# Performance work log

Measured on AMD Instinct MI355X. Metric: run time of the kernel, lower is better.

Reference implementation:

```python
import jax, jax.numpy as jnp
import numpy as np
from jax import lax

N, C, H, W, Q, HD = 2, 64, 96, 96, 147456, 128

def make_coord(h, w):
    # pixel-center coords in [-1,1]; channel 0 -> H dim, channel 1 -> W dim
    y = -1.0 + (2.0 * jnp.arange(h) + 1.0) / h
    x = -1.0 + (2.0 * jnp.arange(w) + 1.0) / w
    yy, xx = jnp.meshgrid(y, x, indexing='ij')
    return jnp.stack([yy, xx], 0)[None]  # [1,2,h,w]

def _pix(c, n):
    # align_corners=False unnormalization
    return ((c + 1.0) * n - 1.0) / 2.0

def gather_nearest(img, cy, cx):
    # img [n,c,h,w]; cy,cx [n,q] in [-1,1] -> [n,q,c]
    n, c, h, w = img.shape
    iy = jnp.clip(jnp.round(_pix(cy, h)).astype(jnp.int32), 0, h - 1)
    ix = jnp.clip(jnp.round(_pix(cx, w)).astype(jnp.int32), 0, w - 1)
    flat = img.reshape(n, c, h * w)
    out = jnp.take_along_axis(flat, (iy * w + ix)[:, None, :], axis=2)
    return out.transpose(0, 2, 1)

def sample_bilinear_border(img, cy, cx):
    # grid_sample bilinear, padding_mode='border', align_corners=False
    n, c, h, w = img.shape
    fy = jnp.clip(_pix(cy, h), 0.0, h - 1.0)
    fx = jnp.clip(_pix(cx, w), 0.0, w - 1.0)
    y0 = jnp.floor(fy); x0 = jnp.floor(fx)
    wy = fy - y0; wx = fx - x0
    y0i = jnp.clip(y0.astype(jnp.int32), 0, h - 1); y1i = jnp.clip(y0i + 1, 0, h - 1)
    x0i = jnp.clip(x0.astype(jnp.int32), 0, w - 1); x1i = jnp.clip(x0i + 1, 0, w - 1)
    flat = img.reshape(n, c, h * w)
    def g(iy, ix):
        return jnp.take_along_axis(flat, (iy * w + ix)[:, None, :], axis=2)
    v = (g(y0i, x0i) * ((1 - wy) * (1 - wx))[:, None, :]
         + g(y0i, x1i) * ((1 - wy) * wx)[:, None, :]
         + g(y1i, x0i) * (wy * (1 - wx))[:, None, :]
         + g(y1i, x1i) * (wy * wx)[:, None, :])
    return v.transpose(0, 2, 1)

def mlp3(x, w1, b1, w2, b2, w3, b3):
    hdd = jax.nn.relu(x @ w1 + b1)
    hdd = jax.nn.relu(hdd @ w2 + b2)
    return hdd @ w3 + b3

def posenc(rel, hd):
    # sinusoid PE: 2 coord dims x (sin,cos) x hd//4 octave bands -> hd feats
    f = (2.0 ** jnp.arange(hd // 4)) * jnp.pi
    ang = rel[..., None] * f  # [n,q,2,hd//4]
    n, q = rel.shape[:2]
    return jnp.concatenate([jnp.sin(ang), jnp.cos(ang)], -1).reshape(n, q, hd)

def reference(lr, feat, raw_disp, coord, cell, coef_w, coef_b, freq_w, freq_b, phase_w,
              im_w1, im_b1, im_w2, im_b2, im_w3, im_b3,
              dp_w1, dp_b1, dp_w2, dp_b2, dp_w3, dp_b3):
    n, c, h, w = feat.shape
    hd = coef_b.shape[0]
    conv = lambda x, wk, bk: lax.conv_general_dilated(
        x, wk, (1, 1), 'SAME', dimension_numbers=('NCHW', 'OIHW', 'NCHW')) + bk[None, :, None, None]
    coef = conv(feat, coef_w, coef_b)
    freq = conv(feat, freq_w, freq_b)
    scale = 2.0 / (cell + 1e-6)[:, 0, 1] / w  # [n]
    disp = raw_disp * scale[:, None, None, None]
    mean_d = jnp.mean(disp, (1, 2, 3), keepdims=True)
    std_d = jnp.std(disp, (1, 2, 3), keepdims=True, ddof=1) + 1e-6
    dnorm = (disp - mean_d) / std_d
    rx, ry = 1.0 / h, 1.0 / w  # 2/dim/2
    fcoord = jnp.broadcast_to(make_coord(h, w), (n, 2, h, w))
    hw = jnp.array([h, w], coord.dtype)
    phase = (cell * hw) @ phase_w  # [n,q,hd]
    preds, pdisps, areas = [], [], []
    for vx in (-1, 1):
        for vy in (-1, 1):
            cy = jnp.clip(coord[:, :, 0] + vx * rx + 1e-6, -1 + 1e-6, 1 - 1e-6)
            cx = jnp.clip(coord[:, :, 1] + vy * ry + 1e-6, -1 + 1e-6, 1 - 1e-6)
            q_disp = gather_nearest(dnorm, cy, cx)   # [n,q,1]
            q_inp = gather_nearest(feat, cy, cx)     # [n,q,c]
            q_coef = gather_nearest(coef, cy, cx)    # [n,q,hd]
            q_freq = gather_nearest(freq, cy, cx)    # [n,q,hd]
            q_coord = gather_nearest(fcoord, cy, cx) # [n,q,2]
            rel = (coord - q_coord) * hw
            coord_ff = posenc(rel, hd)
            pdisps.append(mlp3(jnp.concatenate([q_disp, q_inp, rel], -1),
                               dp_w1, dp_b1, dp_w2, dp_b2, dp_w3, dp_b3))
            qf = q_freq * coord_ff + phase
            preds.append(mlp3(q_coef * qf, im_w1, im_b1, im_w2, im_b2, im_w3, im_b3))
            areas.append(jnp.abs(rel[:, :, 0] * rel[:, :, 1]) + 1e-9)
    tot = areas[0] + areas[1] + areas[2] + areas[3]
    order = [3, 2, 1, 0]  # local-ensemble diagonal area swap
    ret = sum(preds[i] * (areas[order[i]] / tot)[..., None] for i in range(4))
    ret_d = sum(pdisps[i] * (areas[order[i]] / tot)[..., None] for i in range(4))
    cy, cx = coord[:, :, 0], coord[:, :, 1]
    rgb = ret + sample_bilinear_border(lr, cy, cx)
    out_disp = ret_d + sample_bilinear_border(disp, cy, cx)
    return jnp.concatenate([rgb, out_disp], -1)  # [n,q,4]

def setup_inputs() -> dict:
    key = jax.random.key(0)
    ks = jax.random.split(key, 16)
    s = 0.02
    return {
        'lr': jax.random.uniform(ks[0], (N, 3, H, W), jnp.float32),
        'feat': jax.random.normal(ks[1], (N, C, H, W), jnp.float32),
        'raw_disp': jax.random.normal(ks[2], (N, 1, H, W), jnp.float32),
        'coord': jax.random.uniform(ks[3], (N, Q, 2), jnp.float32) * 2.0 - 1.0,
        'cell': jnp.full((N, Q, 2), 2.0 / 384.0, jnp.float32),
        'coef_w': jax.random.normal(ks[4], (HD, C, 3, 3), jnp.float32) * s,
        'coef_b': jnp.zeros((HD,), jnp.float32),
        'freq_w': jax.random.normal(ks[5], (HD, C, 3, 3), jnp.float32) * s,
        'freq_b': jnp.zeros((HD,), jnp.float32),
        'phase_w': jax.random.normal(ks[6], (2, HD), jnp.float32) * s,
        'im_w1': jax.random.normal(ks[7], (HD, 256), jnp.float32) * s,
        'im_b1': jnp.zeros((256,), jnp.float32),
        'im_w2': jax.random.normal(ks[8], (256, 256), jnp.float32) * s,
        'im_b2': jnp.zeros((256,), jnp.float32),
        'im_w3': jax.random.normal(ks[9], (256, 3), jnp.float32) * s,
        'im_b3': jnp.zeros((3,), jnp.float32),
        'dp_w1': jax.random.normal(ks[10], (C + 3, 256), jnp.float32) * s,
        'dp_b1': jnp.zeros((256,), jnp.float32),
        'dp_w2': jax.random.normal(ks[11], (256, 256), jnp.float32) * s,
        'dp_b2': jnp.zeros((256,), jnp.float32),
        'dp_w3': jax.random.normal(ks[12], (256, 1), jnp.float32) * s,
        'dp_b3': jnp.zeros((1,), jnp.float32),
    }
```

## Files before the change

kernel.cpp:

```cpp
#include <hip/hip_runtime.h>

#define QTOT 147456

typedef __attribute__((ext_vector_type(8))) short bf16x8;
typedef __attribute__((ext_vector_type(8))) unsigned short u16x8;
typedef __attribute__((ext_vector_type(4))) float f32x4;

union V8 { u16x8 v; unsigned short us[8]; };

__device__ __forceinline__ unsigned short f2b(float f){
  unsigned int u = __float_as_uint(f);
  return (unsigned short)((u + 0x7fffu + ((u >> 16) & 1u)) >> 16);
}
__device__ __forceinline__ float b2f(unsigned short s){
  return __uint_as_float(((unsigned int)s) << 16);
}
__device__ __forceinline__ unsigned cvtpk(float lo, float hi){
  unsigned r;
  asm("v_cvt_pk_bf16_f32 %0, %1, %2" : "=v"(r) : "v"(lo), "v"(hi));
  return r;
}

#define OFF_STATS   0
#define OFF_FPAD    256
#define OFF_SAMP    (OFF_FPAD + 2458624)
#define OFF_DNORM   (OFF_SAMP + 589824)
#define OFF_COEFT   (OFF_DNORM + 73728)
#define OFF_FREQT   (OFF_COEFT + 4718592)
#define OFF_WIM1    (OFF_FREQT + 4718592)
#define OFF_WIM2    (OFF_WIM1 + 65536)
#define OFF_WIM3    (OFF_WIM2 + 131072)
#define OFF_WDP1    (OFF_WIM3 + 8192)
#define OFF_WDP2    (OFF_WDP1 + 49152)
#define OFF_WDP3    (OFF_WDP2 + 131072)
#define OFF_WCV     (OFF_WDP3 + 8192)

__global__ void kStats(const float* __restrict__ raw_disp, const float* __restrict__ cell,
                       float* __restrict__ stats){
  int n = blockIdx.x;
  float cellv = cell[((size_t)n*QTOT)*2 + 1];
  float scale = 2.0f/(cellv + 1e-6f)/96.0f;
  __shared__ double sd[256], sq[256];
  double s=0.0, s2=0.0;
  for(int i=threadIdx.x;i<9216;i+=256){
    float d = raw_disp[(size_t)n*9216 + i]*scale;
    double dd = (double)d; s += dd; s2 += dd*dd;
  }
  sd[threadIdx.x]=s; sq[threadIdx.x]=s2; __syncthreads();
  for(int o=128;o>0;o>>=1){
    if(threadIdx.x<o){ sd[threadIdx.x]+=sd[threadIdx.x+o]; sq[threadIdx.x]+=sq[threadIdx.x+o]; }
    __syncthreads();
  }
  if(threadIdx.x==0){
    double mean = sd[0]/9216.0;
    double var  = (sq[0] - sd[0]*sd[0]/9216.0)/9215.0;
    if(var < 0.0) var = 0.0;
    stats[n*2+0] = (float)mean;
    stats[n*2+1] = (float)sqrt(var) + 1e-6f;
  }
}

__global__ void kPackImgs(const float* __restrict__ feat, const float* __restrict__ lr,
                          const float* __restrict__ raw_disp, const float* __restrict__ cell,
                          const float* __restrict__ stats,
                          unsigned short* __restrict__ featPad, float* __restrict__ sampT,
                          float* __restrict__ dnormT){
  int i = blockIdx.x*256 + threadIdx.x;
  if(i >= 2*98*98) return;
  int n = i/(98*98); int remi = i%(98*98);
  int py = remi/98, px = remi%98;
  bool inter = (py>=1 && py<=96 && px>=1 && px<=96);
  int y = py-1, x = px-1;
  for(int cb=0;cb<8;cb++){
    V8 v;
    #pragma unroll
    for(int e=0;e<8;e++){
      int c = cb*8+e;
      float f = inter ? feat[(((size_t)n*64 + c)*96 + y)*96 + x] : 0.0f;
      v.us[e] = f2b(f);
    }
    *(u16x8*)(featPad + (size_t)i*64 + cb*8) = v.v;
  }
  if(inter){
    float cellv = cell[((size_t)n*QTOT)*2 + 1];
    float scale = 2.0f/(cellv + 1e-6f)/96.0f;
    float d = raw_disp[((size_t)n*96 + y)*96 + x]*scale;
    size_t p = (size_t)n*9216 + y*96 + x;
    float4 sv;
    sv.x = lr[(((size_t)n*3 + 0)*96 + y)*96 + x];
    sv.y = lr[(((size_t)n*3 + 1)*96 + y)*96 + x];
    sv.z = lr[(((size_t)n*3 + 2)*96 + y)*96 + x];
    sv.w = d;
    *(float4*)(sampT + p*4) = sv;
    dnormT[p] = (d - stats[n*2+0]) / stats[n*2+1];
  }
}

__device__ __forceinline__ void packKN(unsigned short* dst, const float* src,
                                       int K, int N, int Npad, int i){
  int j = i & 7; int tt = i >> 3;
  int col = tt % Npad; tt /= Npad;
  int qq = tt & 3; int kc = tt >> 2;
  int k = kc*32 + qq*8 + j;
  float v = (k < K && col < N) ? src[(size_t)k*N + col] : 0.0f;
  dst[i] = f2b(v);
}

__global__ void kPackW(const float* im_w1, const float* im_w2, const float* im_w3,
                       const float* dp_w1, const float* dp_w2, const float* dp_w3,
                       const float* coef_w, const float* freq_w,
                       unsigned short* wIm1, unsigned short* wIm2, unsigned short* wIm3,
                       unsigned short* wDp1, unsigned short* wDp2, unsigned short* wDp3,
                       unsigned short* wCv){
  int i = blockIdx.x*256 + threadIdx.x;
  if(i < 32768){ packKN(wIm1, im_w1, 128, 256, 256, i); return; } i -= 32768;
  if(i < 65536){ packKN(wIm2, im_w2, 256, 256, 256, i); return; } i -= 65536;
  if(i < 4096){  packKN(wIm3, im_w3, 256, 3, 16, i);    return; } i -= 4096;
  if(i < 24576){
    int j = i & 7; int tt = i >> 3;
    int col = tt % 256; tt /= 256;
    int qq = tt & 3; int kc = tt >> 2;
    int kn = kc*32 + qq*8 + j;
    int ko = (kn < 64) ? kn + 1 : ((kn == 64) ? 0 : kn);
    float v = (kn < 67) ? dp_w1[(size_t)ko*256 + col] : 0.0f;
    wDp1[i] = f2b(v);
    return;
  } i -= 24576;
  if(i < 65536){ packKN(wDp2, dp_w2, 256, 256, 256, i); return; } i -= 65536;
  if(i < 4096){  packKN(wDp3, dp_w3, 256, 1, 16, i);    return; } i -= 4096;
  if(i < 147456){
    int ii = i;
    int j = ii & 7; int tt = ii >> 3;
    int col = tt % 128; tt /= 128;
    int qq = tt & 3; tt >>= 2;
    int kc = tt & 1; tt >>= 1;
    int tap = tt % 9; int z = tt / 9;
    int k = kc*32 + qq*8 + j;
    const float* w = z ? freq_w : coef_w;
    wCv[i] = f2b(w[((size_t)col*64 + k)*9 + tap]);
  }
}

__global__ __launch_bounds__(512) void kConv(const unsigned short* __restrict__ featPad,
                                             const unsigned short* __restrict__ wCv,
                                             const float* __restrict__ coef_b,
                                             const float* __restrict__ freq_b,
                                             unsigned short* __restrict__ coefT,
                                             unsigned short* __restrict__ freqT){
  int bx = blockIdx.x;
  int y  = blockIdx.y;
  int nz = blockIdx.z; int n = nz >> 1, z = nz & 1;
  const unsigned short* wp = wCv + (size_t)z*73728;
  const float* bias = z ? freq_b : coef_b;
  unsigned short* dst = z ? freqT : coefT;
  int t = threadIdx.x, lane = t & 63, w = t >> 6;
  int x0 = bx*48;
  int colBase = w*16 + (lane & 15);
  int qq = lane >> 4;
  f32x4 acc[3] = {};
  #pragma unroll
  for(int tap=0;tap<9;tap++){
    int ky = tap/3, kx = tap%3;
    #pragma unroll
    for(int kc=0;kc<2;kc++){
      bf16x8 bfr = *(const bf16x8*)(wp + (((size_t)(tap*2 + kc)*4 + qq)*128 + colBase)*8);
      #pragma unroll
      for(int mt=0;mt<3;mt++){
        int pxi = x0 + mt*16 + (lane & 15) + kx;
        int pyi = y + ky;
        const unsigned short* ap = featPad + (((size_t)n*98 + pyi)*98 + pxi)*64 + kc*32 + qq*8;
        bf16x8 afr = *(const bf16x8*)ap;
        acc[mt] = __builtin_amdgcn_mfma_f32_16x16x32_bf16(afr, bfr, acc[mt], 0, 0, 0);
      }
    }
  }
  float bv = bias[colBase];
  #pragma unroll
  for(int mt=0;mt<3;mt++){
    #pragma unroll
    for(int j=0;j<4;j++){
      int px = x0 + mt*16 + (lane>>4)*4 + j;
      dst[((size_t)n*9216 + y*96 + px)*128 + colBase] = f2b(acc[mt][j] + bv);
    }
  }
}

#define H1B 0u
#define XB  16384u
#define H2B 16384u

__global__ __launch_bounds__(256, 4) void kMega(
    const float* __restrict__ coord, const float* __restrict__ cell,
    const float* __restrict__ phase_w,
    const float* __restrict__ im_b1, const float* __restrict__ im_b2, const float* __restrict__ im_b3,
    const float* __restrict__ dp_b1, const float* __restrict__ dp_b2, const float* __restrict__ dp_b3,
    const unsigned short* __restrict__ coefT, const unsigned short* __restrict__ freqT,
    const unsigned short* __restrict__ featPad, const float* __restrict__ dnormT,
    const float* __restrict__ sampT,
    const unsigned short* __restrict__ wIm1, const unsigned short* __restrict__ wIm2,
    const unsigned short* __restrict__ wIm3,
    const unsigned short* __restrict__ wDp1, const unsigned short* __restrict__ wDp2,
    const unsigned short* __restrict__ wDp3,
    float* __restrict__ out){
  __shared__ __align__(128) char smem[32768];
  __shared__ float2 sPhW2[128];
  __shared__ int   sIy[32], sIx[32], sFoff[32];
  __shared__ float sRelY[32], sRelX[32], sArea[32], sPc0[32], sPc1[32];
  __shared__ unsigned short sXs[32*8];
  __shared__ float sPredIm[128], sPredDp[32];

  const int b = blockIdx.x;
  const int n = b / 18432;
  const int q0 = (b % 18432) * 8;
  const int t = threadIdx.x;
  const int lane = t & 63;
  const int w = t >> 6;

  if(t < 128){
    sPhW2[((t & 15) << 3) | (t >> 4)] = make_float2(phase_w[t], phase_w[128 + t]);
  }
  if(t < 32){
    int r = t;
    int q = q0 + (r >> 2); int v = r & 3;
    float vx = (v & 2) ? 1.0f : -1.0f;
    float vy = (v & 1) ? 1.0f : -1.0f;
    size_t ci = ((size_t)n*QTOT + q)*2;
    float cyo = coord[ci], cxo = coord[ci+1];
    const float RX = 1.0f/96.0f;
    float lo = -1.0f + 1e-6f, hi = 1.0f - 1e-6f;
    float cy = fminf(fmaxf(cyo + vx*RX + 1e-6f, lo), hi);
    float cx = fminf(fmaxf(cxo + vy*RX + 1e-6f, lo), hi);
    float fpy = ((cy + 1.0f)*96.0f - 1.0f)*0.5f;
    float fpx = ((cx + 1.0f)*96.0f - 1.0f)*0.5f;
    int iy = (int)rintf(fpy); iy = iy < 0 ? 0 : (iy > 95 ? 95 : iy);
    int ix = (int)rintf(fpx); ix = ix < 0 ? 0 : (ix > 95 ? 95 : ix);
    float qcy = -1.0f + (2.0f*(float)iy + 1.0f)/96.0f;
    float qcx = -1.0f + (2.0f*(float)ix + 1.0f)/96.0f;
    float ry = (cyo - qcy)*96.0f;
    float rx = (cxo - qcx)*96.0f;
    sIy[r]=iy; sIx[r]=ix; sRelY[r]=ry; sRelX[r]=rx;
    sArea[r] = fabsf(ry*rx) + 1e-9f;
    sFoff[r] = ((n*98 + iy + 1)*98 + (ix + 1))*64;
    float2 cl = *(const float2*)(cell + ci);
    sPc0[r] = cl.x * 96.0f; sPc1[r] = cl.y * 96.0f;
    float qd = dnormT[(size_t)n*9216 + iy*96 + ix];
    V8 xr;
    #pragma unroll
    for(int e=0;e<8;++e) xr.us[e] = 0;
    xr.us[0] = f2b(qd); xr.us[1] = f2b(ry); xr.us[2] = f2b(rx);
    *(u16x8*)(sXs + r*8) = xr.v;
  }
  __syncthreads();

  {
    int r = t >> 3, h8 = t & 7;
    int c0 = h8 * 16;
    float rel = (c0 < 64) ? sRelY[r] : sRelX[r];
    bool isCos = (c0 & 32) != 0;
    float rp = rel * 3.14159265358979323846f;
    double rev0 = (double)rp * 0.15915494309189535;
    double rf = rev0 - floor(rev0);
    unsigned long long F = (unsigned long long)(rf * 18446744073709551616.0);
    if(c0 & 16) F <<= 16;
    float pc0 = sPc0[r], pc1 = sPc1[r];
    int pix = sIy[r]*96 + sIx[r];
    const unsigned short* cp = coefT + ((size_t)n*9216 + pix)*128 + c0;
    const unsigned short* fp = freqT + ((size_t)n*9216 + pix)*128 + c0;
    unsigned rowb = XB + (unsigned)r*256u;
    for(int it=0; it<2; ++it){
      V8 qc, qf, ov;
      qc.v = *(const u16x8*)(cp + it*8);
      qf.v = *(const u16x8*)(fp + it*8);
      float xv[8];
      #pragma unroll
      for(int e=0;e<8;++e){
        float fv = (float)(unsigned)(F >> 32) * 0x1p-32f;
        float ff = isCos ? __builtin_amdgcn_cosf(fv) : __builtin_amdgcn_sinf(fv);
        F += F;
        float2 pw = sPhW2[(it*8 + e)*8 + h8];
        float ph = pc0*pw.x + pc1*pw.y;
        xv[e] = b2f(qc.us[e]) * (b2f(qf.us[e])*ff + ph);
      }
      unsigned* ow = (unsigned*)&ov;
      ow[0] = cvtpk(xv[0], xv[1]); ow[1] = cvtpk(xv[2], xv[3]);
      ow[2] = cvtpk(xv[4], xv[5]); ow[3] = cvtpk(xv[6], xv[7]);
      int ch = h8*2 + it;
      *(u16x8*)(smem + rowb + ((unsigned)(ch ^ (r & 7)) << 4)) = ov.v;
    }
  }
  __syncthreads();

  auto layerT = [&](int nkc, unsigned aBase, int aSh, const unsigned short* wp,
                    const float* bias, unsigned oBase){
    const int wn = w;
    f32x4 acc[2][4] = {};
    for(int kc=0; kc<nkc; ++kc){
      int ch = kc*4 + (lane >> 4);
      bf16x8 af[2], wf[4];
      #pragma unroll
      for(int mt=0; mt<2; ++mt){
        int r = mt*16 + (lane & 15);
        af[mt] = *(const bf16x8*)(smem + aBase + ((unsigned)r << aSh)
                                  + ((unsigned)(ch ^ (r & 7)) << 4));
      }
      #pragma unroll
      for(int nt=0; nt<4; ++nt){
        int col = wn*64 + nt*16 + (lane & 15);
        wf[nt] = *(const bf16x8*)(wp + ((size_t)ch*256 + col)*8);
      }
      #pragma unroll
      for(int mt=0; mt<2; ++mt)
        #pragma unroll
        for(int nt=0; nt<4; ++nt)
          acc[mt][nt] = __builtin_amdgcn_mfma_f32_16x16x32_bf16(wf[nt], af[mt], acc[mt][nt], 0,0,0);
    }
    #pragma unroll
    for(int nt=0; nt<4; ++nt){
      int n0 = wn*64 + nt*16 + (lane>>4)*4;
      float4 bv = *(const float4*)(bias + n0);
      #pragma unroll
      for(int mt=0; mt<2; ++mt){
        int r = mt*16 + (lane & 15);
        float h0 = fmaxf(acc[mt][nt][0] + bv.x, 0.0f);
        float h1 = fmaxf(acc[mt][nt][1] + bv.y, 0.0f);
        float h2 = fmaxf(acc[mt][nt][2] + bv.z, 0.0f);
        float h3 = fmaxf(acc[mt][nt][3] + bv.w, 0.0f);
        uint2 pv;
        pv.x = cvtpk(h0, h1);
        pv.y = cvtpk(h2, h3);
        *(uint2*)(smem + oBase + (unsigned)r*512u
                  + ((unsigned)(((n0>>3) ^ (r & 7))) << 4)
                  + (unsigned)((n0 & 7) << 1)) = pv;
      }
    }
  };

  auto layerDp1 = [&](const unsigned short* wp, const float* bias, unsigned oBase){
    const int wn = w;
    f32x4 acc[2][4] = {};
    int fo0 = sFoff[lane & 15];
    int fo1 = sFoff[16 + (lane & 15)];
    #pragma unroll
    for(int kc=0; kc<3; ++kc){
      int ch = kc*4 + (lane >> 4);
      bf16x8 af[2], wf[4];
      if(kc < 2){
        int csub = kc*32 + (lane >> 4)*8;
        af[0] = *(const bf16x8*)(featPad + fo0 + csub);
        af[1] = *(const bf16x8*)(featPad + fo1 + csub);
      } else {
        af[0] = bf16x8{}; af[1] = bf16x8{};
        if((lane >> 4) == 0){
          af[0] = *(const bf16x8*)(sXs + (lane & 15)*8);
          af[1] = *(const bf16x8*)(sXs + (16 + (lane & 15))*8);
        }
      }
      #pragma unroll
      for(int nt=0; nt<4; ++nt){
        int col = wn*64 + nt*16 + (lane & 15);
        wf[nt] = *(const bf16x8*)(wp + ((size_t)ch*256 + col)*8);
      }
      #pragma unroll
      for(int mt=0; mt<2; ++mt)
        #pragma unroll
        for(int nt=0; nt<4; ++nt)
          acc[mt][nt] = __builtin_amdgcn_mfma_f32_16x16x32_bf16(wf[nt], af[mt], acc[mt][nt], 0,0,0);
    }
    #pragma unroll
    for(int nt=0; nt<4; ++nt){
      int n0 = wn*64 + nt*16 + (lane>>4)*4;
      float4 bv = *(const float4*)(bias + n0);
      #pragma unroll
      for(int mt=0; mt<2; ++mt){
        int r = mt*16 + (lane & 15);
        float h0 = fmaxf(acc[mt][nt][0] + bv.x, 0.0f);
        float h1 = fmaxf(acc[mt][nt][1] + bv.y, 0.0f);
        float h2 = fmaxf(acc[mt][nt][2] + bv.z, 0.0f);
        float h3 = fmaxf(acc[mt][nt][3] + bv.w, 0.0f);
        uint2 pv;
        pv.x = cvtpk(h0, h1);
        pv.y = cvtpk(h2, h3);
        *(uint2*)(smem + oBase + (unsigned)r*512u
                  + ((unsigned)(((n0>>3) ^ (r & 7))) << 4)
                  + (unsigned)((n0 & 7) << 1)) = pv;
      }
    }
  };

  auto layerOut = [&](const unsigned short* wp, float b30, float b31, float b32, bool isIm){
    if(w < 2){
      int mt = w;
      f32x4 acc = {};
      for(int kc=0; kc<8; ++kc){
        int ch = kc*4 + (lane >> 4);
        int r = mt*16 + (lane & 15);
        bf16x8 a  = *(const bf16x8*)(smem + H2B + (unsigned)r*512u
                                     + ((unsigned)(ch ^ (r & 7)) << 4));
        bf16x8 bb = *(const bf16x8*)(wp + ((size_t)ch*16 + (lane & 15))*8);
        acc = __builtin_amdgcn_mfma_f32_16x16x32_bf16(bb, a, acc, 0,0,0);
      }
      if(lane < 16){
        int row = mt*16 + lane;
        if(isIm){
          sPredIm[row*4+0] = acc[0] + b30;
          sPredIm[row*4+1] = acc[1] + b31;
          sPredIm[row*4+2] = acc[2] + b32;
        } else {
          sPredDp[row] = acc[0] + b30;
        }
      }
    }
  };

  float ib0 = im_b3[0], ib1 = im_b3[1], ib2 = im_b3[2];
  float db0 = dp_b3[0];

  layerT(4, XB, 8, wIm1, im_b1, H1B);   __syncthreads();
  layerT(8, H1B, 9, wIm2, im_b2, H2B);  __syncthreads();
  layerOut(wIm3, ib0, ib1, ib2, true);  __syncthreads();

  layerDp1(wDp1, dp_b1, H1B);           __syncthreads();
  layerT(8, H1B, 9, wDp2, dp_b2, H2B);  __syncthreads();
  layerOut(wDp3, db0, 0.0f, 0.0f, false); __syncthreads();

  if(t < 32){
    int ql = t >> 2, ch = t & 3;
    int rb = ql*4;
    float a0=sArea[rb], a1=sArea[rb+1], a2=sArea[rb+2], a3=sArea[rb+3];
    float tot = a0 + a1 + a2 + a3;
    float w0=a3/tot, w1=a2/tot, w2=a1/tot, w3=a0/tot;
    float ret;
    if(ch < 3)
      ret = sPredIm[(rb+0)*4+ch]*w0 + sPredIm[(rb+1)*4+ch]*w1
          + sPredIm[(rb+2)*4+ch]*w2 + sPredIm[(rb+3)*4+ch]*w3;
    else
      ret = sPredDp[rb+0]*w0 + sPredDp[rb+1]*w1 + sPredDp[rb+2]*w2 + sPredDp[rb+3]*w3;
    int q = q0 + ql;
    size_t ci = ((size_t)n*QTOT + q)*2;
    float cy = coord[ci], cx = coord[ci+1];
    float fy = fminf(fmaxf(((cy + 1.0f)*96.0f - 1.0f)*0.5f, 0.0f), 95.0f);
    float fx = fminf(fmaxf(((cx + 1.0f)*96.0f - 1.0f)*0.5f, 0.0f), 95.0f);
    float y0f = floorf(fy), x0f = floorf(fx);
    float wy = fy - y0f, wx = fx - x0f;
    int y0i = (int)y0f; int x0i = (int)x0f;
    int y1i = y0i + 1 > 95 ? 95 : y0i + 1;
    int x1i = x0i + 1 > 95 ? 95 : x0i + 1;
    const float* sp = sampT + (size_t)n*9216*4;
    float v00 = sp[((size_t)y0i*96 + x0i)*4 + ch];
    float v01 = sp[((size_t)y0i*96 + x1i)*4 + ch];
    float v10 = sp[((size_t)y1i*96 + x0i)*4 + ch];
    float v11 = sp[((size_t)y1i*96 + x1i)*4 + ch];
    float samp = v00*((1.0f-wy)*(1.0f-wx)) + v01*((1.0f-wy)*wx)
               + v10*(wy*(1.0f-wx)) + v11*(wy*wx);
    out[((size_t)n*QTOT + q)*4 + ch] = ret + samp;
  }
}

extern "C" void kernel_launch(void* const* d_in, const int* in_sizes, int n_in,
                              void* d_out, int out_size, void* d_ws, size_t ws_size,
                              hipStream_t stream){
  const float* lr       = (const float*)d_in[0];
  const float* feat     = (const float*)d_in[1];
  const float* raw_disp = (const float*)d_in[2];
  const float* coord    = (const float*)d_in[3];
  const float* cell     = (const float*)d_in[4];
  const float* coef_w   = (const float*)d_in[5];
  const float* coef_b   = (const float*)d_in[6];
  const float* freq_w   = (const float*)d_in[7];
  const float* freq_b   = (const float*)d_in[8];
  const float* phase_w  = (const float*)d_in[9];
  const float* im_w1    = (const float*)d_in[10];
  const float* im_b1    = (const float*)d_in[11];
  const float* im_w2    = (const float*)d_in[12];
  const float* im_b2    = (const float*)d_in[13];
  const float* im_w3    = (const float*)d_in[14];
  const float* im_b3    = (const float*)d_in[15];
  const float* dp_w1    = (const float*)d_in[16];
  const float* dp_b1    = (const float*)d_in[17];
  const float* dp_w2    = (const float*)d_in[18];
  const float* dp_b2    = (const float*)d_in[19];
  const float* dp_w3    = (const float*)d_in[20];
  const float* dp_b3    = (const float*)d_in[21];

  char* ws = (char*)d_ws;
  float* stats            = (float*)(ws + OFF_STATS);
  unsigned short* featPad = (unsigned short*)(ws + OFF_FPAD);
  float* sampT            = (float*)(ws + OFF_SAMP);
  float* dnormT           = (float*)(ws + OFF_DNORM);
  unsigned short* coefT   = (unsigned short*)(ws + OFF_COEFT);
  unsigned short* freqT   = (unsigned short*)(ws + OFF_FREQT);
  unsigned short* wIm1    = (unsigned short*)(ws + OFF_WIM1);
  unsigned short* wIm2    = (unsigned short*)(ws + OFF_WIM2);
  unsigned short* wIm3    = (unsigned short*)(ws + OFF_WIM3);
  unsigned short* wDp1    = (unsigned short*)(ws + OFF_WDP1);
  unsigned short* wDp2    = (unsigned short*)(ws + OFF_WDP2);
  unsigned short* wDp3    = (unsigned short*)(ws + OFF_WDP3);
  unsigned short* wCv     = (unsigned short*)(ws + OFF_WCV);
  float* out = (float*)d_out;

  kStats<<<2, 256, 0, stream>>>(raw_disp, cell, stats);
  kPackImgs<<<(2*98*98 + 255)/256, 256, 0, stream>>>(feat, lr, raw_disp, cell, stats,
                                                     featPad, sampT, dnormT);
  kPackW<<<(344064 + 255)/256, 256, 0, stream>>>(im_w1, im_w2, im_w3, dp_w1, dp_w2, dp_w3,
                                                 coef_w, freq_w,
                                                 wIm1, wIm2, wIm3, wDp1, wDp2, wDp3, wCv);
  kConv<<<dim3(2, 96, 4), 512, 0, stream>>>(featPad, wCv, coef_b, freq_b, coefT, freqT);

  kMega<<<36864, 256, 0, stream>>>(coord, cell, phase_w,
                                   im_b1, im_b2, im_b3, dp_b1, dp_b2, dp_b3,
                                   coefT, freqT, featPad, dnormT, sampT,
                                   wIm1, wIm2, wIm3, wDp1, wDp2, wDp3, out);
}
```

Before: 730.8 us.

## Fuse MLP output layer into second hidden layer epilogue and shrink LDS

After: 1.289 ms. 76.4% more time.

```diff
diff --git a/kernel.cpp b/kernel.cpp
--- a/kernel.cpp
+++ b/kernel.cpp
@@ -34,6 +34,8 @@
 #define OFF_WDP2    (OFF_WDP1 + 49152)
 #define OFF_WDP3    (OFF_WDP2 + 131072)
 #define OFF_WCV     (OFF_WDP3 + 8192)
+#define OFF_W3IMT   (OFF_WCV + 294912)
+#define OFF_W3DPT   (OFF_W3IMT + 3072)
 
 __global__ void kStats(const float* __restrict__ raw_disp, const float* __restrict__ cell,
                        float* __restrict__ stats){
@@ -109,13 +111,12 @@
 __global__ void kPackW(const float* im_w1, const float* im_w2, const float* im_w3,
                        const float* dp_w1, const float* dp_w2, const float* dp_w3,
                        const float* coef_w, const float* freq_w,
-                       unsigned short* wIm1, unsigned short* wIm2, unsigned short* wIm3,
-                       unsigned short* wDp1, unsigned short* wDp2, unsigned short* wDp3,
-                       unsigned short* wCv){
+                       unsigned short* wIm1, unsigned short* wIm2,
+                       unsigned short* wDp1, unsigned short* wDp2,
+                       unsigned short* wCv, float* w3imT, float* w3dpT){
   int i = blockIdx.x*256 + threadIdx.x;
   if(i < 32768){ packKN(wIm1, im_w1, 128, 256, 256, i); return; } i -= 32768;
   if(i < 65536){ packKN(wIm2, im_w2, 256, 256, 256, i); return; } i -= 65536;
-  if(i < 4096){  packKN(wIm3, im_w3, 256, 3, 16, i);    return; } i -= 4096;
   if(i < 24576){
     int j = i & 7; int tt = i >> 3;
     int col = tt % 256; tt /= 256;
@@ -127,7 +128,6 @@
     return;
   } i -= 24576;
   if(i < 65536){ packKN(wDp2, dp_w2, 256, 256, 256, i); return; } i -= 65536;
-  if(i < 4096){  packKN(wDp3, dp_w3, 256, 1, 16, i);    return; } i -= 4096;
   if(i < 147456){
     int ii = i;
     int j = ii & 7; int tt = ii >> 3;
@@ -138,7 +138,10 @@
     int k = kc*32 + qq*8 + j;
     const float* w = z ? freq_w : coef_w;
     wCv[i] = f2b(w[((size_t)col*64 + k)*9 + tap]);
-  }
+    return;
+  } i -= 147456;
+  if(i < 768){ w3imT[i] = im_w3[(size_t)(i & 255)*3 + (i >> 8)]; return; } i -= 768;
+  if(i < 256){ w3dpT[i] = dp_w3[i]; }
 }
 
 __global__ __launch_bounds__(512) void kConv(const unsigned short* __restrict__ featPad,
@@ -187,9 +190,8 @@
 
 #define H1B 0u
 #define XB  16384u
-#define H2B 16384u
-
-__global__ __launch_bounds__(256, 4) void kMega(
+
+__global__ __launch_bounds__(256, 6) void kMega(
     const float* __restrict__ coord, const float* __restrict__ cell,
     const float* __restrict__ phase_w,
     const float* __restrict__ im_b1, const float* __restrict__ im_b2, const float* __restrict__ im_b3,
@@ -198,16 +200,16 @@
     const unsigned short* __restrict__ featPad, const float* __restrict__ dnormT,
     const float* __restrict__ sampT,
     const unsigned short* __restrict__ wIm1, const unsigned short* __restrict__ wIm2,
-    const unsigned short* __restrict__ wIm3,
     const unsigned short* __restrict__ wDp1, const unsigned short* __restrict__ wDp2,
-    const unsigned short* __restrict__ wDp3,
+    const float* __restrict__ w3imT, const float* __restrict__ w3dpT,
     float* __restrict__ out){
-  __shared__ __align__(128) char smem[32768];
-  __shared__ float2 sPhW2[128];
-  __shared__ int   sIy[32], sIx[32], sFoff[32];
+  __shared__ __align__(128) char smem[24576];
+  __shared__ int   sPix[32], sFoff[32];
   __shared__ float sRelY[32], sRelX[32], sArea[32], sPc0[32], sPc1[32];
   __shared__ unsigned short sXs[32*8];
-  __shared__ float sPredIm[128], sPredDp[32];
+
+  float2* sPhW2 = (float2*)(smem + H1B);
+  float*  sPart = (float*)(smem + XB);
 
   const int b = blockIdx.x;
   const int n = b / 18432;
@@ -238,7 +240,8 @@
     float qcx = -1.0f + (2.0f*(float)ix + 1.0f)/96.0f;
     float ry = (cyo - qcy)*96.0f;
     float rx = (cxo - qcx)*96.0f;
-    sIy[r]=iy; sIx[r]=ix; sRelY[r]=ry; sRelX[r]=rx;
+    sPix[r] = iy*96 + ix;
+    sRelY[r]=ry; sRelX[r]=rx;
     sArea[r] = fabsf(ry*rx) + 1e-9f;
     sFoff[r] = ((n*98 + iy + 1)*98 + (ix + 1))*64;
     float2 cl = *(const float2*)(cell + ci);
@@ -263,7 +266,7 @@
     unsigned long long F = (unsigned long long)(rf * 18446744073709551616.0);
     if(c0 & 16) F <<= 16;
     float pc0 = sPc0[r], pc1 = sPc1[r];
-    int pix = sIy[r]*96 + sIx[r];
+    int pix = sPix[r];
     const unsigned short* cp = coefT + ((size_t)n*9216 + pix)*128 + c0;
     const unsigned short* fp = freqT + ((size_t)n*9216 + pix)*128 + c0;
     unsigned rowb = XB + (unsigned)r*256u;
@@ -387,54 +390,92 @@
     }
   };
 
-  auto layerOut = [&](const unsigned short* wp, float b30, float b31, float b32, bool isIm){
-    if(w < 2){
-      int mt = w;
-      f32x4 acc = {};
-      for(int kc=0; kc<8; ++kc){
-        int ch = kc*4 + (lane >> 4);
+  auto layerL2f = [&](const unsigned short* wp, const float* bias,
+                      const float* w3t, int nc){
+    const int wn = w;
+    f32x4 acc[2][4] = {};
+    for(int kc=0; kc<8; ++kc){
+      int ch = kc*4 + (lane >> 4);
+      bf16x8 af[2], wf[4];
+      #pragma unroll
+      for(int mt=0; mt<2; ++mt){
         int r = mt*16 + (lane & 15);
-        bf16x8 a  = *(const bf16x8*)(smem + H2B + (unsigned)r*512u
-                                     + ((unsigned)(ch ^ (r & 7)) << 4));
-        bf16x8 bb = *(const bf16x8*)(wp + ((size_t)ch*16 + (lane & 15))*8);
-        acc = __builtin_amdgcn_mfma_f32_16x16x32_bf16(bb, a, acc, 0,0,0);
-      }
-      if(lane < 16){
-        int row = mt*16 + lane;
-        if(isIm){
-          sPredIm[row*4+0] = acc[0] + b30;
-          sPredIm[row*4+1] = acc[1] + b31;
-          sPredIm[row*4+2] = acc[2] + b32;
-        } else {
-          sPredDp[row] = acc[0] + b30;
+        af[mt] = *(const bf16x8*)(smem + H1B + ((unsigned)r << 9)
+                                  + ((unsigned)(ch ^ (r & 7)) << 4));
+      }
+      #pragma unroll
+      for(int nt=0; nt<4; ++nt){
+        int col = wn*64 + nt*16 + (lane & 15);
+        wf[nt] = *(const bf16x8*)(wp + ((size_t)ch*256 + col)*8);
+      }
+      #pragma unroll
+      for(int mt=0; mt<2; ++mt)
+        #pragma unroll
+        for(int nt=0; nt<4; ++nt)
+          acc[mt][nt] = __builtin_amdgcn_mfma_f32_16x16x32_bf16(wf[nt], af[mt], acc[mt][nt], 0,0,0);
+    }
+    float part[2][3] = {};
+    #pragma unroll
+    for(int nt=0; nt<4; ++nt){
+      int n0 = wn*64 + nt*16 + (lane>>4)*4;
+      float4 bv = *(const float4*)(bias + n0);
+      float4 wv[3];
+      wv[0] = *(const float4*)(w3t + n0);
+      if(nc == 3){
+        wv[1] = *(const float4*)(w3t + 256 + n0);
+        wv[2] = *(const float4*)(w3t + 512 + n0);
+      }
+      #pragma unroll
+      for(int mt=0; mt<2; ++mt){
+        float h0 = fmaxf(acc[mt][nt][0] + bv.x, 0.0f);
+        float h1 = fmaxf(acc[mt][nt][1] + bv.y, 0.0f);
+        float h2 = fmaxf(acc[mt][nt][2] + bv.z, 0.0f);
+        float h3 = fmaxf(acc[mt][nt][3] + bv.w, 0.0f);
+        part[mt][0] += h0*wv[0].x + h1*wv[0].y + h2*wv[0].z + h3*wv[0].w;
+        if(nc == 3){
+          part[mt][1] += h0*wv[1].x + h1*wv[1].y + h2*wv[1].z + h3*wv[1].w;
+          part[mt][2] += h0*wv[2].x + h1*wv[2].y + h2*wv[2].z + h3*wv[2].w;
         }
       }
     }
+    #pragma unroll
+    for(int mt=0; mt<2; ++mt){
+      #pragma unroll
+      for(int c=0; c<3; ++c){
+        if(c < nc){
+          float v = part[mt][c];
+          v += __shfl_xor(v, 16, 64);
+          v += __shfl_xor(v, 32, 64);
+          if(lane < 16){
+            int slot = (nc == 3) ? c : 3;
+            sPart[((w*32) + mt*16 + lane)*4 + slot] = v;
+          }
+        }
+      }
+    }
   };
 
-  float ib0 = im_b3[0], ib1 = im_b3[1], ib2 = im_b3[2];
-  float db0 = dp_b3[0];
-
-  layerT(4, XB, 8, wIm1, im_b1, H1B);   __syncthreads();
-  layerT(8, H1B, 9, wIm2, im_b2, H2B);  __syncthreads();
-  layerOut(wIm3, ib0, ib1, ib2, true);  __syncthreads();
-
-  layerDp1(wDp1, dp_b1, H1B);           __syncthreads();
-  layerT(8, H1B, 9, wDp2, dp_b2, H2B);  __syncthreads();
-  layerOut(wDp3, db0, 0.0f, 0.0f, false); __syncthreads();
+  layerT(4, XB, 8, wIm1, im_b1, H1B);     __syncthreads();
+  layerL2f(wIm2, im_b2, w3imT, 3);        __syncthreads();
+
+  layerDp1(wDp1, dp_b1, H1B);             __syncthreads();
+  layerL2f(wDp2, dp_b2, w3dpT, 1);        __syncthreads();
 
   if(t < 32){
     int ql = t >> 2, ch = t & 3;
     int rb = ql*4;
+    float b3 = (ch < 3) ? im_b3[ch] : dp_b3[0];
+    float p[4];
+    #pragma unroll
+    for(int k=0;k<4;++k){
+      int r = rb + k;
+      p[k] = sPart[(r)*4 + ch] + sPart[(32 + r)*4 + ch]
+           + sPart[(64 + r)*4 + ch] + sPart[(96 + r)*4 + ch] + b3;
+    }
     float a0=sArea[rb], a1=sArea[rb+1], a2=sArea[rb+2], a3=sArea[rb+3];
     float tot = a0 + a1 + a2 + a3;
     float w0=a3/tot, w1=a2/tot, w2=a1/tot, w3=a0/tot;
-    float ret;
-    if(ch < 3)
-      ret = sPredIm[(rb+0)*4+ch]*w0 + sPredIm[(rb+1)*4+ch]*w1
-          + sPredIm[(rb+2)*4+ch]*w2 + sPredIm[(rb+3)*4+ch]*w3;
-    else
-      ret = sPredDp[rb+0]*w0 + sPredDp[rb+1]*w1 + sPredDp[rb+2]*w2 + sPredDp[rb+3]*w3;
+    float ret = p[0]*w0 + p[1]*w1 + p[2]*w2 + p[3]*w3;
     int q = q0 + ql;
     size_t ci = ((size_t)n*QTOT + q)*2;
     float cy = coord[ci], cx = coord[ci+1];
@@ -491,23 +532,23 @@
   unsigned short* freqT   = (unsigned short*)(ws + OFF_FREQT);
   unsigned short* wIm1    = (unsigned short*)(ws + OFF_WIM1);
   unsigned short* wIm2    = (unsigned short*)(ws + OFF_WIM2);
-  unsigned short* wIm3    = (unsigned short*)(ws + OFF_WIM3);
   unsigned short* wDp1    = (unsigned short*)(ws + OFF_WDP1);
   unsigned short* wDp2    = (unsigned short*)(ws + OFF_WDP2);
-  unsigned short* wDp3    = (unsigned short*)(ws + OFF_WDP3);
   unsigned short* wCv     = (unsigned short*)(ws + OFF_WCV);
+  float* w3imT            = (float*)(ws + OFF_W3IMT);
+  float* w3dpT            = (float*)(ws + OFF_W3DPT);
   float* out = (float*)d_out;
 
   kStats<<<2, 256, 0, stream>>>(raw_disp, cell, stats);
   kPackImgs<<<(2*98*98 + 255)/256, 256, 0, stream>>>(feat, lr, raw_disp, cell, stats,
                                                      featPad, sampT, dnormT);
-  kPackW<<<(344064 + 255)/256, 256, 0, stream>>>(im_w1, im_w2, im_w3, dp_w1, dp_w2, dp_w3,
+  kPackW<<<(345088 + 255)/256, 256, 0, stream>>>(im_w1, im_w2, im_w3, dp_w1, dp_w2, dp_w3,
                                                  coef_w, freq_w,
-                                                 wIm1, wIm2, wIm3, wDp1, wDp2, wDp3, wCv);
+                                                 wIm1, wIm2, wDp1, wDp2, wCv, w3imT, w3dpT);
   kConv<<<dim3(2, 96, 4), 512, 0, stream>>>(featPad, wCv, coef_b, freq_b, coefT, freqT);
 
   kMega<<<36864, 256, 0, stream>>>(coord, cell, phase_w,
                                    im_b1, im_b2, im_b3, dp_b1, dp_b2, dp_b3,
                                    coefT, freqT, featPad, dnormT, sampT,
-                                   wIm1, wIm2, wIm3, wDp1, wDp2, wDp3, out);
-}
+                                   wIm1, wIm2, wDp1, wDp2, w3imT, w3dpT, out);
+}
```

## Run hidden MLP layers in FP8 MFMA and halve LDS footprint

Applied to the files above, without the earlier changes.

Measured after the change: 879.5 us. 1.2x slower.

```diff
diff --git a/kernel.cpp b/kernel.cpp
--- a/kernel.cpp
+++ b/kernel.cpp
@@ -19,6 +19,17 @@
   unsigned r;
   asm("v_cvt_pk_bf16_f32 %0, %1, %2" : "=v"(r) : "v"(lo), "v"(hi));
   return r;
+}
+__device__ __forceinline__ unsigned pk4fp8(float a, float b, float c, float d){
+  unsigned lo = 0, hi = 0;
+  asm("v_cvt_pk_fp8_f32 %0, %1, %2" : "+v"(lo) : "v"(a), "v"(b));
+  asm("v_cvt_pk_fp8_f32 %0, %1, %2" : "+v"(hi) : "v"(c), "v"(d));
+  return (lo & 0xffffu) | (hi << 16);
+}
+__device__ __forceinline__ unsigned char f2fp8(float v){
+  unsigned r = 0;
+  asm("v_cvt_pk_fp8_f32 %0, %1, %2" : "+v"(r) : "v"(v), "v"(v));
+  return (unsigned char)(r & 0xffu);
 }
 
 #define OFF_STATS   0
@@ -29,11 +40,11 @@
 #define OFF_FREQT   (OFF_COEFT + 4718592)
 #define OFF_WIM1    (OFF_FREQT + 4718592)
 #define OFF_WIM2    (OFF_WIM1 + 65536)
-#define OFF_WIM3    (OFF_WIM2 + 131072)
-#define OFF_WDP1    (OFF_WIM3 + 8192)
+#define OFF_WIM3    (OFF_WIM2 + 65536)
+#define OFF_WDP1    (OFF_WIM3 + 4096)
 #define OFF_WDP2    (OFF_WDP1 + 49152)
-#define OFF_WDP3    (OFF_WDP2 + 131072)
-#define OFF_WCV     (OFF_WDP3 + 8192)
+#define OFF_WDP3    (OFF_WDP2 + 65536)
+#define OFF_WCV     (OFF_WDP3 + 4096)
 
 __global__ void kStats(const float* __restrict__ raw_disp, const float* __restrict__ cell,
                        float* __restrict__ stats){
@@ -105,17 +116,26 @@
   float v = (k < K && col < N) ? src[(size_t)k*N + col] : 0.0f;
   dst[i] = f2b(v);
 }
+__device__ __forceinline__ void packKN8(unsigned char* dst, const float* src,
+                                        int K, int N, int Npad, int i){
+  int j = i & 7; int tt = i >> 3;
+  int col = tt % Npad; tt /= Npad;
+  int qq = tt & 3; int kc = tt >> 2;
+  int k = kc*32 + qq*8 + j;
+  float v = (k < K && col < N) ? src[(size_t)k*N + col] : 0.0f;
+  dst[i] = f2fp8(v);
+}
 
 __global__ void kPackW(const float* im_w1, const float* im_w2, const float* im_w3,
                        const float* dp_w1, const float* dp_w2, const float* dp_w3,
                        const float* coef_w, const float* freq_w,
-                       unsigned short* wIm1, unsigned short* wIm2, unsigned short* wIm3,
-                       unsigned short* wDp1, unsigned short* wDp2, unsigned short* wDp3,
+                       unsigned short* wIm1, unsigned char* wIm2, unsigned char* wIm3,
+                       unsigned short* wDp1, unsigned char* wDp2, unsigned char* wDp3,
                        unsigned short* wCv){
   int i = blockIdx.x*256 + threadIdx.x;
   if(i < 32768){ packKN(wIm1, im_w1, 128, 256, 256, i); return; } i -= 32768;
-  if(i < 65536){ packKN(wIm2, im_w2, 256, 256, 256, i); return; } i -= 65536;
-  if(i < 4096){  packKN(wIm3, im_w3, 256, 3, 16, i);    return; } i -= 4096;
+  if(i < 65536){ packKN8(wIm2, im_w2, 256, 256, 256, i); return; } i -= 65536;
+  if(i < 4096){  packKN8(wIm3, im_w3, 256, 3, 16, i);    return; } i -= 4096;
   if(i < 24576){
     int j = i & 7; int tt = i >> 3;
     int col = tt % 256; tt /= 256;
@@ -126,8 +146,8 @@
     wDp1[i] = f2b(v);
     return;
   } i -= 24576;
-  if(i < 65536){ packKN(wDp2, dp_w2, 256, 256, 256, i); return; } i -= 65536;
-  if(i < 4096){  packKN(wDp3, dp_w3, 256, 1, 16, i);    return; } i -= 4096;
+  if(i < 65536){ packKN8(wDp2, dp_w2, 256, 256, 256, i); return; } i -= 65536;
+  if(i < 4096){  packKN8(wDp3, dp_w3, 256, 1, 16, i);    return; } i -= 4096;
   if(i < 147456){
     int ii = i;
     int j = ii & 7; int tt = ii >> 3;
@@ -186,8 +206,8 @@
 }
 
 #define H1B 0u
-#define XB  16384u
-#define H2B 16384u
+#define XB  8192u
+#define H2B 8192u
 
 __global__ __launch_bounds__(256, 4) void kMega(
     const float* __restrict__ coord, const float* __restrict__ cell,
@@ -197,17 +217,18 @@
     const unsigned short* __restrict__ coefT, const unsigned short* __restrict__ freqT,
     const unsigned short* __restrict__ featPad, const float* __restrict__ dnormT,
     const float* __restrict__ sampT,
-    const unsigned short* __restrict__ wIm1, const unsigned short* __restrict__ wIm2,
-    const unsigned short* __restrict__ wIm3,
-    const unsigned short* __restrict__ wDp1, const unsigned short* __restrict__ wDp2,
-    const unsigned short* __restrict__ wDp3,
+    const unsigned short* __restrict__ wIm1, const unsigned char* __restrict__ wIm2,
+    const unsigned char* __restrict__ wIm3,
+    const unsigned short* __restrict__ wDp1, const unsigned char* __restrict__ wDp2,
+    const unsigned char* __restrict__ wDp3,
     float* __restrict__ out){
-  __shared__ __align__(128) char smem[32768];
-  __shared__ float2 sPhW2[128];
-  __shared__ int   sIy[32], sIx[32], sFoff[32];
+  __shared__ __align__(128) char smem[16384];
+  __shared__ int   sPix[32], sFoff[32];
   __shared__ float sRelY[32], sRelX[32], sArea[32], sPc0[32], sPc1[32];
   __shared__ unsigned short sXs[32*8];
   __shared__ float sPredIm[128], sPredDp[32];
+
+  float2* sPhW2 = (float2*)(smem + H1B);
 
   const int b = blockIdx.x;
   const int n = b / 18432;
@@ -238,7 +259,8 @@
     float qcx = -1.0f + (2.0f*(float)ix + 1.0f)/96.0f;
     float ry = (cyo - qcy)*96.0f;
     float rx = (cxo - qcx)*96.0f;
-    sIy[r]=iy; sIx[r]=ix; sRelY[r]=ry; sRelX[r]=rx;
+    sPix[r] = iy*96 + ix;
+    sRelY[r]=ry; sRelX[r]=rx;
     sArea[r] = fabsf(ry*rx) + 1e-9f;
     sFoff[r] = ((n*98 + iy + 1)*98 + (ix + 1))*64;
     float2 cl = *(const float2*)(cell + ci);
@@ -263,7 +285,7 @@
     unsigned long long F = (unsigned long long)(rf * 18446744073709551616.0);
     if(c0 & 16) F <<= 16;
     float pc0 = sPc0[r], pc1 = sPc1[r];
-    int pix = sIy[r]*96 + sIx[r];
+    int pix = sPix[r];
     const unsigned short* cp = coefT + ((size_t)n*9216 + pix)*128 + c0;
     const unsigned short* fp = freqT + ((size_t)n*9216 + pix)*128 + c0;
     unsigned rowb = XB + (unsigned)r*256u;
@@ -290,23 +312,27 @@
   }
   __syncthreads();
 
-  auto layerT = [&](int nkc, unsigned aBase, int aSh, const unsigned short* wp,
-                    const float* bias, unsigned oBase){
+  auto h8store = [&](unsigned base, int r, int n0, unsigned pv){
+    *(unsigned*)(smem + base + (unsigned)r*256u
+                 + ((unsigned)(((n0 >> 3) ^ (r & 7))) << 3) + (unsigned)(n0 & 7)) = pv;
+  };
+
+  auto layerL1im = [&](){
     const int wn = w;
     f32x4 acc[2][4] = {};
-    for(int kc=0; kc<nkc; ++kc){
+    for(int kc=0; kc<4; ++kc){
       int ch = kc*4 + (lane >> 4);
       bf16x8 af[2], wf[4];
       #pragma unroll
       for(int mt=0; mt<2; ++mt){
         int r = mt*16 + (lane & 15);
-        af[mt] = *(const bf16x8*)(smem + aBase + ((unsigned)r << aSh)
+        af[mt] = *(const bf16x8*)(smem + XB + (unsigned)r*256u
                                   + ((unsigned)(ch ^ (r & 7)) << 4));
       }
       #pragma unroll
       for(int nt=0; nt<4; ++nt){
         int col = wn*64 + nt*16 + (lane & 15);
-        wf[nt] = *(const bf16x8*)(wp + ((size_t)ch*256 + col)*8);
+        wf[nt] = *(const bf16x8*)(wIm1 + ((size_t)ch*256 + col)*8);
       }
       #pragma unroll
       for(int mt=0; mt<2; ++mt)
@@ -317,25 +343,20 @@
     #pragma unroll
     for(int nt=0; nt<4; ++nt){
       int n0 = wn*64 + nt*16 + (lane>>4)*4;
-      float4 bv = *(const float4*)(bias + n0);
+      float4 bv = *(const float4*)(im_b1 + n0);
       #pragma unroll
       for(int mt=0; mt<2; ++mt){
         int r = mt*16 + (lane & 15);
-        float h0 = fmaxf(acc[mt][nt][0] + bv.x, 0.0f);
-        float h1 = fmaxf(acc[mt][nt][1] + bv.y, 0.0f);
-        float h2 = fmaxf(acc[mt][nt][2] + bv.z, 0.0f);
-        float h3 = fmaxf(acc[mt][nt][3] + bv.w, 0.0f);
-        uint2 pv;
-        pv.x = cvtpk(h0, h1);
-        pv.y = cvtpk(h2, h3);
-        *(uint2*)(smem + oBase + (unsigned)r*512u
-                  + ((unsigned)(((n0>>3) ^ (r & 7))) << 4)
-                  + (unsigned)((n0 & 7) << 1)) = pv;
+        unsigned pv = pk4fp8(fmaxf(acc[mt][nt][0] + bv.x, 0.0f),
+                             fmaxf(acc[mt][nt][1] + bv.y, 0.0f),
+                             fmaxf(acc[mt][nt][2] + bv.z, 0.0f),
+                             fmaxf(acc[mt][nt][3] + bv.w, 0.0f));
+        h8store(H1B, r, n0, pv);
       }
     }
   };
 
-  auto layerDp1 = [&](const unsigned short* wp, const float* bias, unsigned oBase){
+  auto layerDp1 = [&](){
     const int wn = w;
     f32x4 acc[2][4] = {};
     int fo0 = sFoff[lane & 15];
@@ -358,7 +379,7 @@
       #pragma unroll
       for(int nt=0; nt<4; ++nt){
         int col = wn*64 + nt*16 + (lane & 15);
-        wf[nt] = *(const bf16x8*)(wp + ((size_t)ch*256 + col)*8);
+        wf[nt] = *(const bf16x8*)(wDp1 + ((size_t)ch*256 + col)*8);
       }
       #pragma unroll
       for(int mt=0; mt<2; ++mt)
@@ -369,35 +390,70 @@
     #pragma unroll
     for(int nt=0; nt<4; ++nt){
       int n0 = wn*64 + nt*16 + (lane>>4)*4;
-      float4 bv = *(const float4*)(bias + n0);
+      float4 bv = *(const float4*)(dp_b1 + n0);
       #pragma unroll
       for(int mt=0; mt<2; ++mt){
         int r = mt*16 + (lane & 15);
-        float h0 = fmaxf(acc[mt][nt][0] + bv.x, 0.0f);
-        float h1 = fmaxf(acc[mt][nt][1] + bv.y, 0.0f);
-        float h2 = fmaxf(acc[mt][nt][2] + bv.z, 0.0f);
-        float h3 = fmaxf(acc[mt][nt][3] + bv.w, 0.0f);
-        uint2 pv;
-        pv.x = cvtpk(h0, h1);
-        pv.y = cvtpk(h2, h3);
-        *(uint2*)(smem + oBase + (unsigned)r*512u
-                  + ((unsigned)(((n0>>3) ^ (r & 7))) << 4)
-                  + (unsigned)((n0 & 7) << 1)) = pv;
+        unsigned pv = pk4fp8(fmaxf(acc[mt][nt][0] + bv.x, 0.0f),
+                             fmaxf(acc[mt][nt][1] + bv.y, 0.0f),
+                             fmaxf(acc[mt][nt][2] + bv.z, 0.0f),
+                             fmaxf(acc[mt][nt][3] + bv.w, 0.0f));
+        h8store(H1B, r, n0, pv);
       }
     }
   };
 
-  auto layerOut = [&](const unsigned short* wp, float b30, float b31, float b32, bool isIm){
+  auto layerF8 = [&](const unsigned char* __restrict__ wp8, const float* __restrict__ bias){
+    const int wn = w;
+    f32x4 acc[2][4] = {};
+    for(int kc=0; kc<8; ++kc){
+      int ch = kc*4 + (lane >> 4);
+      long long af[2], wf[4];
+      #pragma unroll
+      for(int mt=0; mt<2; ++mt){
+        int r = mt*16 + (lane & 15);
+        af[mt] = *(const long long*)(smem + H1B + (unsigned)r*256u
+                                     + ((unsigned)(ch ^ (r & 7)) << 3));
+      }
+      #pragma unroll
+      for(int nt=0; nt<4; ++nt){
+        int col = wn*64 + nt*16 + (lane & 15);
+        wf[nt] = *(const long long*)(wp8 + ((size_t)ch*256 + col)*8);
+      }
+      #pragma unroll
+      for(int mt=0; mt<2; ++mt)
+        #pragma unroll
+        for(int nt=0; nt<4; ++nt)
+          acc[mt][nt] = __builtin_amdgcn_mfma_f32_16x16x32_fp8_fp8(wf[nt], af[mt], acc[mt][nt], 0,0,0);
+    }
+    #pragma unroll
+    for(int nt=0; nt<4; ++nt){
+      int n0 = wn*64 + nt*16 + (lane>>4)*4;
+      float4 bv = *(const float4*)(bias + n0);
+      #pragma unroll
+      for(int mt=0; mt<2; ++mt){
+        int r = mt*16 + (lane & 15);
+        unsigned pv = pk4fp8(fmaxf(acc[mt][nt][0] + bv.x, 0.0f),
+                             fmaxf(acc[mt][nt][1] + bv.y, 0.0f),
+                             fmaxf(acc[mt][nt][2] + bv.z, 0.0f),
+                             fmaxf(acc[mt][nt][3] + bv.w, 0.0f));
+        h8store(H2B, r, n0, pv);
+      }
+    }
+  };
+
+  auto layerOutF8 = [&](const unsigned char* __restrict__ wp8,
+                        float b30, float b31, float b32, bool isIm){
     if(w < 2){
       int mt = w;
       f32x4 acc = {};
       for(int kc=0; kc<8; ++kc){
         int ch = kc*4 + (lane >> 4);
         int r = mt*16 + (lane & 15);
-        bf16x8 a  = *(const bf16x8*)(smem + H2B + (unsigned)r*512u
-                                     + ((unsigned)(ch ^ (r & 7)) << 4));
-        bf16x8 bb = *(const bf16x8*)(wp + ((size_t)ch*16 + (lane & 15))*8);
-        acc = __builtin_amdgcn_mfma_f32_16x16x32_bf16(bb, a, acc, 0,0,0);
+        long long a  = *(const long long*)(smem + H2B + (unsigned)r*256u
+                                           + ((unsigned)(ch ^ (r & 7)) << 3));
+        long long bb = *(const long long*)(wp8 + ((size_t)ch*16 + (lane & 15))*8);
+        acc = __builtin_amdgcn_mfma_f32_16x16x32_fp8_fp8(bb, a, acc, 0,0,0);
       }
       if(lane < 16){
         int row = mt*16 + lane;
@@ -415,13 +471,13 @@
   float ib0 = im_b3[0], ib1 = im_b3[1], ib2 = im_b3[2];
   float db0 = dp_b3[0];
 
-  layerT(4, XB, 8, wIm1, im_b1, H1B);   __syncthreads();
-  layerT(8, H1B, 9, wIm2, im_b2, H2B);  __syncthreads();
-  layerOut(wIm3, ib0, ib1, ib2, true);  __syncthreads();
-
-  layerDp1(wDp1, dp_b1, H1B);           __syncthreads();
-  layerT(8, H1B, 9, wDp2, dp_b2, H2B);  __syncthreads();
-  layerOut(wDp3, db0, 0.0f, 0.0f, false); __syncthreads();
+  layerL1im();                              __syncthreads();
+  layerF8(wIm2, im_b2);                     __syncthreads();
+  layerOutF8(wIm3, ib0, ib1, ib2, true);    __syncthreads();
+
+  layerDp1();                               __syncthreads();
+  layerF8(wDp2, dp_b2);                     __syncthreads();
+  layerOutF8(wDp3, db0, 0.0f, 0.0f, false); __syncthreads();
 
   if(t < 32){
     int ql = t >> 2, ch = t & 3;
@@ -490,11 +546,11 @@
   unsigned short* coefT   = (unsigned short*)(ws + OFF_COEFT);
   unsigned short* freqT   = (unsigned short*)(ws + OFF_FREQT);
   unsigned short* wIm1    = (unsigned short*)(ws + OFF_WIM1);
-  unsigned short* wIm2    = (unsigned short*)(ws + OFF_WIM2);
-  unsigned short* wIm3    = (unsigned short*)(ws + OFF_WIM3);
+  unsigned char* wIm2     = (unsigned char*)(ws + OFF_WIM2);
+  unsigned char* wIm3     = (unsigned char*)(ws + OFF_WIM3);
   unsigned short* wDp1    = (unsigned short*)(ws + OFF_WDP1);
-  unsigned short* wDp2    = (unsigned short*)(ws + OFF_WDP2);
-  unsigned short* wDp3    = (unsigned short*)(ws + OFF_WDP3);
+  unsigned char* wDp2     = (unsigned char*)(ws + OFF_WDP2);
+  unsigned char* wDp3     = (unsigned char*)(ws + OFF_WDP3);
   unsigned short* wCv     = (unsigned short*)(ws + OFF_WCV);
   float* out = (float*)d_out;
 
```
